# Kernel optimization log

Hardware: AMD Instinct MI355X
Metric: run time of the kernel (lower is better)

## Reference

```python
import jax, jax.numpy as jnp
import numpy as np

# ---- static structure for the 28x28 image grid ----
H = 28
V = H * H          # 784 vertices
T = 25             # landscape sample points
K_MAX = 2          # landscape orders kept
M0 = 0.05          # DTM mass parameter

_idx = np.arange(V).reshape(H, H)
_e_h = np.stack([_idx[:, :-1].ravel(), _idx[:, 1:].ravel()], 1)
_e_v = np.stack([_idx[:-1, :].ravel(), _idx[1:, :].ravel()], 1)
EDGES = np.concatenate([_e_h, _e_v], 0).astype(np.int32)   # [E,2], E=1512
E = EDGES.shape[0]

# grid coordinates per lims=[[27,0],[0,27]], normalized to [0,1]
_c0 = np.linspace(1.0, 0.0, H)
_c1 = np.linspace(0.0, 1.0, H)
COORDS = np.stack(np.meshgrid(_c0, _c1, indexing='ij'), -1).reshape(V, 2)
_D2 = ((COORDS[:, None, :] - COORDS[None, :, :]) ** 2).sum(-1)   # [V,V] static
ORDER = jnp.asarray(np.argsort(_D2, 1).astype(np.int32))          # nearest-first per row
D2S = jnp.asarray(np.take_along_axis(_D2, np.argsort(_D2, 1), 1).astype(np.float32))
TSEQ = jnp.asarray(np.linspace(0.0, 0.5, T).astype(np.float32))   # landscape eval grid
EA = jnp.asarray(EDGES[:, 0])
EB = jnp.asarray(EDGES[:, 1])


def _dtm(w):
    """Distance-to-measure filtration on the grid. w: [B,V] pixel masses -> [B,V]."""
    m = w / jnp.clip(jnp.sum(w, 1, keepdims=True), 1e-12)
    ws = m[:, ORDER]                                  # [B,V,V] masses in nearest-first order
    c = jnp.cumsum(ws, -1)
    take = jnp.minimum(ws, jnp.clip(M0 - (c - ws), 0.0, None))  # mass used until m0 reached
    return jnp.sqrt(jnp.sum(take * D2S[None], -1) / M0 + 1e-12)


def _ph0(f):
    """0-dim persistence of sublevel filtration of f on the grid graph (Kruskal/union-find).
    f: [V] -> (births, deaths, valid) each [E]."""
    w = jnp.maximum(f[EA], f[EB])                     # edge filtration values
    o = jnp.argsort(w)
    aa, bb, ww = EA[o], EB[o], w[o]

    def step(carry, e):
        r, bv = carry                                 # r: fully-compressed root per vertex
        ai, bi, wi = e
        ra, rb = r[ai], r[bi]
        diff = ra != rb
        young_a = bv[ra] >= bv[rb]                    # younger comp = larger birth
        young = jnp.where(young_a, ra, rb)
        old = jnp.where(young_a, rb, ra)
        birth = bv[young]
        r = jnp.where(diff & (r == young), old, r)    # merge, keep full compression
        return (r, bv), (birth, wi, diff)

    init = (jnp.arange(V, dtype=jnp.int32), f)
    _, (bs, ds, valid) = jax.lax.scan(step, init, (aa, bb, ww))
    return bs, ds, valid


def _landscape(bs, ds, valid):
    """Persistence landscape lambda_k(t), k<K_MAX, t in TSEQ -> [K_MAX*T] features."""
    tent = jnp.maximum(jnp.minimum(TSEQ[:, None] - bs[None, :], ds[None, :] - TSEQ[:, None]), 0.0)
    tent = tent * valid[None, :]                      # [T,E]
    top = jax.lax.top_k(tent, K_MAX)[0]               # [T,K]
    return top.T.reshape(-1)                          # [K*T] = 50


def setup_inputs() -> dict:
    key = jax.random.key(0)
    k1, k2, k3, k4, k5 = jax.random.split(key, 5)
    return {
        'input': jax.random.uniform(k1, (128, 1, 28, 28), dtype=jnp.float32),
        'w_topo': jax.random.normal(k2, (50, 100), dtype=jnp.float32) * 0.1,
        'b_topo': jax.random.normal(k3, (100,), dtype=jnp.float32) * 0.01,
        'w_fc': jax.random.normal(k4, (100, 10), dtype=jnp.float32) * 0.1,
        'b_fc': jax.random.normal(k5, (10,), dtype=jnp.float32) * 0.01,
    }


def reference(input, w_topo, b_topo, w_fc, b_fc):
    B = input.shape[0]
    x = input.reshape(B, V)
    f = _dtm(x)                                       # [B,V] DTM filtration
    bs, ds, valid = jax.vmap(_ph0)(f)                 # persistence pairs per sample
    feats = jax.vmap(_landscape)(bs, ds, valid.astype(f.dtype))  # [B,50]
    h = jax.nn.relu(feats @ w_topo + b_topo)          # AdTopoLayer linear + ReLU -> [B,100]
    return h @ w_fc + b_fc                            # [B,10]
```

## Files before the change

kernel.cpp:

```cpp
#include <hip/hip_runtime.h>
#include <math.h>

#define HH 28
#define VV 784
#define EE 1512
#define TT 25
#define M0C 0.05


#define DECODE(idx, A, B)                                                  \
  {                                                                        \
    if ((idx) < 756) {                                                     \
      int i_ = (idx) / 27, j_ = (idx) - i_ * 27;                           \
      A = i_ * HH + j_; B = A + 1;                                         \
    } else {                                                               \
      int q_ = (idx) - 756;                                                \
      int i_ = q_ / HH, j_ = q_ - i_ * HH;                                 \
      A = i_ * HH + j_; B = A + HH;                                        \
    }                                                                      \
  }

__global__ __launch_bounds__(512) void k_sortrows(int* __restrict__ ORDER, float* __restrict__ D2S) {
  __shared__ unsigned long long keys[1024];
  const int v = blockIdx.x;
  const int i1 = v / HH, j1 = v % HH;
  const double step = 1.0 / 27.0;
  const double c0v = (i1 == 27) ? 0.0 : 1.0 - (double)i1 * step;
  const double c1v = (j1 == 27) ? 1.0 : (double)j1 * step;
  for (int u = threadIdx.x; u < 1024; u += 512) {
    unsigned long long key = ~0ULL;
    if (u < VV) {
      int i2 = u / HH, j2 = u % HH;
      double c0u = (i2 == 27) ? 0.0 : 1.0 - (double)i2 * step;
      double c1u = (j2 == 27) ? 1.0 : (double)j2 * step;
      double dx = c0v - c0u, dy = c1v - c1u;
      float d2 = (float)(dx * dx + dy * dy);
      key = ((unsigned long long)__float_as_uint(d2) << 32) | (unsigned)u;
    }
    keys[u] = key;
  }
  __syncthreads();
  for (unsigned k = 2; k <= 1024; k <<= 1) {
    for (unsigned j = k >> 1; j; j >>= 1) {
      for (unsigned i = threadIdx.x; i < 1024; i += 512) {
        unsigned l = i ^ j;
        if (l > i) {
          unsigned long long a = keys[i], c = keys[l];
          if ((a > c) == ((i & k) == 0)) { keys[i] = c; keys[l] = a; }
        }
      }
      __syncthreads();
    }
  }
  for (int u = threadIdx.x; u < VV; u += 512) {
    unsigned long long key = keys[u];
    ORDER[v * VV + u] = (int)(key & 0xffffffffu);
    D2S[v * VV + u] = __uint_as_float((unsigned)(key >> 32));
  }
}

__global__ __launch_bounds__(256) void k_norm(const float* __restrict__ x, float* __restrict__ MT) {
  const int b = blockIdx.x;
  const int tid = threadIdx.x;
  double s = 0.0;
  for (int i = tid; i < VV; i += 256) s += (double)x[b * VV + i];
  for (int off = 32; off; off >>= 1) s += __shfl_xor(s, off, 64);
  __shared__ double sred[4];
  __shared__ double Ssh;
  if ((tid & 63) == 0) sred[tid >> 6] = s;
  __syncthreads();
  if (tid == 0) {
    double S = sred[0] + sred[1] + sred[2] + sred[3];
    Ssh = (S > 1e-12) ? S : 1e-12;
  }
  __syncthreads();
  double S = Ssh;
  for (int i = tid; i < VV; i += 256) MT[i * 128 + b] = (float)((double)x[b * VV + i] / S);
}

__global__ __launch_bounds__(128) void k_dtm(const float* __restrict__ MT, const int* __restrict__ ORDER,
                                             const float* __restrict__ D2S, float* __restrict__ F) {
  const int v = blockIdx.x;
  const int tid = threadIdx.x;
  __shared__ int ordS[VV];
  __shared__ float d2sS[VV];
  for (int k = tid; k < VV; k += 128) {
    ordS[k] = ORDER[v * VV + k];
    d2sS[k] = D2S[v * VV + k];
  }
  __syncthreads();
  float P = 0.0f, acc = 0.0f;
  for (int base = 0; base < VV; base += 16) {
    #pragma unroll
    for (int kk = 0; kk < 16; ++kk) {
      int k = base + kk;
      float mass = MT[ordS[k] * 128 + tid];
      float room = (float)M0C - P;
      room = room > 0.0f ? room : 0.0f;
      float take = mass < room ? mass : room;
      acc += take * d2sS[k];
      P += mass;
    }
    if (__all(P >= (float)M0C)) break;
  }
  F[tid * VV + v] = sqrtf(acc / (float)M0C + 1e-12f);
}

__global__ __launch_bounds__(512) void k_main(const float* __restrict__ F,
                                              const float* __restrict__ w_topo, const float* __restrict__ b_topo,
                                              const float* __restrict__ w_fc, const float* __restrict__ b_fc,
                                              float* __restrict__ out) {
  const int b = blockIdx.x;
  const int tid = threadIdx.x;
  __shared__ float fv[VV];
  __shared__ unsigned long long keys[2048];
  __shared__ unsigned long long par64[VV];
  __shared__ unsigned long long pairs[VV];
  __shared__ float feat[2 * TT];
  __shared__ float hbuf[100];
  __shared__ int cntS;
  for (int i = tid; i < VV; i += 512) {
    float f = F[b * VV + i];
    fv[i] = f;
    par64[i] = ((unsigned long long)__float_as_uint(f) << 32) | (unsigned)i;
  }
  __syncthreads();
  for (int e = tid; e < 2048; e += 512) {
    unsigned long long key = 0xFFFFFFFF00000000ULL;
    if (e < EE) {
      int aa, bb;
      DECODE(e, aa, bb);
      float w = fmaxf(fv[aa], fv[bb]);
      unsigned lo = ((e >= 756) ? (1u << 20) : 0u) | ((unsigned)aa << 10) | (unsigned)bb;
      key = ((unsigned long long)__float_as_uint(w) << 32) | lo;
    }
    keys[e] = key;
  }
  __syncthreads();
  for (unsigned k = 2; k <= 2048; k <<= 1) {
    for (unsigned j = k >> 1; j; j >>= 1) {
      for (unsigned i = tid; i < 2048; i += 512) {
        unsigned l = i ^ j;
        if (l > i) {
          unsigned long long a = keys[i], c = keys[l];
          if ((a > c) == ((i & k) == 0)) { keys[i] = c; keys[l] = a; }
        }
      }
      __syncthreads();
    }
  }
  if (tid < 64) {
    const int lane = tid;
    const unsigned long long lbit = 1ULL << lane;
    int cnt = 0;
    unsigned long long K = keys[lane];
    for (int batch = 0; batch < 24; ++batch) {
      unsigned long long Kn = keys[(batch + 1) * 64 + lane];
      unsigned lo = (unsigned)K;
      int aa = (int)((lo >> 10) & 1023), bb = (int)(lo & 1023);
      unsigned wbits = (unsigned)(K >> 32);
      unsigned long long pka = par64[aa], pkb = par64[bb];
      unsigned ra = (unsigned)pka, rb = (unsigned)pkb;
      unsigned fa = (unsigned)(pka >> 32), fb = (unsigned)(pkb >> 32);
      unsigned long long candB = __ballot(ra != rb);
      if (candB) {
        bool rec = false;
        unsigned long long pairv = 0;
        if (__popcll(candB) == 1) {
          if (ra != rb) {
            bool ya = (fa >= fb);
            unsigned young = ya ? ra : rb;
            unsigned oldv = ya ? rb : ra;
            unsigned foldv = ya ? fb : fa;
            unsigned birth = ya ? fa : fb;
            par64[young] = ((unsigned long long)foldv << 32) | oldv;
            pairv = ((unsigned long long)birth << 32) | wbits;
            rec = (wbits > birth);
          }
        } else {
          int merged = 0;
          unsigned young_w = 0;
          unsigned long long oldpk_w = 0;
          #pragma unroll 4
          for (int j = 0; j < 64; ++j) {
            unsigned s_ra = (unsigned)__builtin_amdgcn_readlane((int)ra, j);
            unsigned s_rb = (unsigned)__builtin_amdgcn_readlane((int)rb, j);
            if (s_ra != s_rb) {
              unsigned s_fa = (unsigned)__builtin_amdgcn_readlane((int)fa, j);
              unsigned s_fb = (unsigned)__builtin_amdgcn_readlane((int)fb, j);
              bool ya = (s_fa >= s_fb);
              unsigned young = ya ? s_ra : s_rb;
              unsigned oldv = ya ? s_rb : s_ra;
              unsigned foldv = ya ? s_fb : s_fa;
              unsigned birth = ya ? s_fa : s_fb;
              bool me = (lane == j);
              merged = me ? 1 : merged;
              young_w = me ? young : young_w;
              oldpk_w = me ? (((unsigned long long)foldv << 32) | oldv) : oldpk_w;
              pairv = me ? (((unsigned long long)birth << 32) | wbits) : pairv;
              bool ma = (ra == young);
              ra = ma ? oldv : ra;
              fa = ma ? foldv : fa;
              bool mb2 = (rb == young);
              rb = mb2 ? oldv : rb;
              fb = mb2 ? foldv : fb;
            }
          }
          if (merged) par64[young_w] = oldpk_w;
          rec = merged && ((unsigned)pairv > (unsigned)(pairv >> 32));
        }
        unsigned long long recB = __ballot(rec);
        int rank = __popcll(recB & (lbit - 1ULL));
        if (rec) pairs[cnt + rank] = pairv;
        cnt += (int)__popcll(recB);
        {
          unsigned long long p[13];
          #pragma unroll
          for (int s = 0; s < 12; ++s) p[s] = par64[lane + 64 * s];
          const int i12 = (lane < 16) ? (768 + lane) : lane;
          p[12] = par64[i12];
          for (;;) {
            bool stable = true;
            #pragma unroll
            for (int s = 0; s < 13; ++s) {
              unsigned r = (unsigned)p[s];
              unsigned long long q = par64[r];
              stable &= ((unsigned)q == r);
              p[s] = q;
            }
            if (__all(stable)) break;
          }
          #pragma unroll
          for (int s = 0; s < 12; ++s) par64[lane + 64 * s] = p[s];
          par64[i12] = p[12];
        }
      }
      K = Kn;
    }
    if (lane == 0) cntS = cnt;
  }
  __syncthreads();
  const int cnt = cntS;
  const int wid = tid >> 6, lane = tid & 63;
  for (int t = wid; t < TT; t += 8) {
    double tvd = (t == 24) ? 0.5 : (double)t * (0.5 / 24.0);
    float tv = (float)tvd;
    float m1 = 0.0f, m2 = 0.0f;
    for (int pidx = lane; pidx < cnt; pidx += 64) {
      unsigned long long pr = pairs[pidx];
      float pbv = __uint_as_float((unsigned)(pr >> 32));
      float pdv = __uint_as_float((unsigned)pr);
      float tent = fminf(tv - pbv, pdv - tv);
      tent = fmaxf(tent, 0.0f);
      if (tent > m1) { m2 = m1; m1 = tent; }
      else if (tent > m2) { m2 = tent; }
    }
    #pragma unroll
    for (int off = 32; off; off >>= 1) {
      float o1 = __shfl_xor(m1, off, 64);
      float o2 = __shfl_xor(m2, off, 64);
      float n1 = fmaxf(m1, o1);
      float n2 = fmaxf(fminf(m1, o1), fmaxf(m2, o2));
      m1 = n1; m2 = n2;
    }
    if (lane == 0) { feat[t] = m1; feat[TT + t] = m2; }
  }
  __syncthreads();
  if (tid < 100) {
    double h = (double)b_topo[tid];
    for (int k2 = 0; k2 < 50; ++k2) h += (double)feat[k2] * (double)w_topo[k2 * 100 + tid];
    hbuf[tid] = (h > 0.0) ? (float)h : 0.0f;
  }
  __syncthreads();
  if (tid < 10) {
    double o = (double)b_fc[tid];
    for (int k2 = 0; k2 < 100; ++k2) o += (double)hbuf[k2] * (double)w_fc[k2 * 10 + tid];
    out[b * 10 + tid] = (float)o;
  }
}

extern "C" void kernel_launch(void* const* d_in, const int* in_sizes, int n_in,
                              void* d_out, int out_size, void* d_ws, size_t ws_size,
                              hipStream_t stream) {
  const float* x = (const float*)d_in[0];
  const float* w_topo = (const float*)d_in[1];
  const float* b_topo = (const float*)d_in[2];
  const float* w_fc = (const float*)d_in[3];
  const float* b_fc = (const float*)d_in[4];
  float* outp = (float*)d_out;
  char* ws = (char*)d_ws;
  int* ORDER = (int*)ws;
  float* D2S = (float*)(ws + 2458624);
  float* MT = (float*)(ws + 4917248);
  float* F = (float*)(ws + 5318656);

  hipLaunchKernelGGL(k_sortrows, dim3(VV), dim3(512), 0, stream, ORDER, D2S);
  hipLaunchKernelGGL(k_norm, dim3(128), dim3(256), 0, stream, x, MT);
  hipLaunchKernelGGL(k_dtm, dim3(VV), dim3(128), 0, stream, MT, ORDER, D2S, F);
  hipLaunchKernelGGL(k_main, dim3(128), dim3(512), 0, stream, F, w_topo, b_topo, w_fc, b_fc, outp);
}
```

Before: 193.7 us.

## Merge sort and normalize kernels; replace pointer-jumping loop with single hop

Folds the row-sort precompute and the per-sample normalization into one launch by giving extra blocks the normalization work, which removes one kernel launch and its dependency gap. In the union-find merge path, the parent entry is now written from the already-updated ra/fa registers instead of a separately tracked packed value. The iterate-until-stable root compression is replaced by a single pointer-jumping hop per vertex. That relies on parent chains never being deeper than two after each merge batch, and it would give wrong roots if that assumption fails.

```diff
diff --git a/kernel.cpp b/kernel.cpp
--- a/kernel.cpp
+++ b/kernel.cpp
@@ -20,62 +20,66 @@
     }                                                                      \
   }
 
-__global__ __launch_bounds__(512) void k_sortrows(int* __restrict__ ORDER, float* __restrict__ D2S) {
+__global__ __launch_bounds__(512) void k_pre(const float* __restrict__ x,
+                                             int* __restrict__ ORDER, float* __restrict__ D2S,
+                                             float* __restrict__ MT) {
   __shared__ unsigned long long keys[1024];
-  const int v = blockIdx.x;
-  const int i1 = v / HH, j1 = v % HH;
-  const double step = 1.0 / 27.0;
-  const double c0v = (i1 == 27) ? 0.0 : 1.0 - (double)i1 * step;
-  const double c1v = (j1 == 27) ? 1.0 : (double)j1 * step;
-  for (int u = threadIdx.x; u < 1024; u += 512) {
-    unsigned long long key = ~0ULL;
-    if (u < VV) {
-      int i2 = u / HH, j2 = u % HH;
-      double c0u = (i2 == 27) ? 0.0 : 1.0 - (double)i2 * step;
-      double c1u = (j2 == 27) ? 1.0 : (double)j2 * step;
-      double dx = c0v - c0u, dy = c1v - c1u;
-      float d2 = (float)(dx * dx + dy * dy);
-      key = ((unsigned long long)__float_as_uint(d2) << 32) | (unsigned)u;
-    }
-    keys[u] = key;
-  }
-  __syncthreads();
-  for (unsigned k = 2; k <= 1024; k <<= 1) {
-    for (unsigned j = k >> 1; j; j >>= 1) {
-      for (unsigned i = threadIdx.x; i < 1024; i += 512) {
-        unsigned l = i ^ j;
-        if (l > i) {
-          unsigned long long a = keys[i], c = keys[l];
-          if ((a > c) == ((i & k) == 0)) { keys[i] = c; keys[l] = a; }
-        }
-      }
-      __syncthreads();
-    }
-  }
-  for (int u = threadIdx.x; u < VV; u += 512) {
-    unsigned long long key = keys[u];
-    ORDER[v * VV + u] = (int)(key & 0xffffffffu);
-    D2S[v * VV + u] = __uint_as_float((unsigned)(key >> 32));
-  }
-}
-
-__global__ __launch_bounds__(256) void k_norm(const float* __restrict__ x, float* __restrict__ MT) {
-  const int b = blockIdx.x;
+  __shared__ double sred[8];
+  __shared__ double Ssh;
   const int tid = threadIdx.x;
-  double s = 0.0;
-  for (int i = tid; i < VV; i += 256) s += (double)x[b * VV + i];
-  for (int off = 32; off; off >>= 1) s += __shfl_xor(s, off, 64);
-  __shared__ double sred[4];
-  __shared__ double Ssh;
-  if ((tid & 63) == 0) sred[tid >> 6] = s;
-  __syncthreads();
-  if (tid == 0) {
-    double S = sred[0] + sred[1] + sred[2] + sred[3];
-    Ssh = (S > 1e-12) ? S : 1e-12;
-  }
-  __syncthreads();
-  double S = Ssh;
-  for (int i = tid; i < VV; i += 256) MT[i * 128 + b] = (float)((double)x[b * VV + i] / S);
+  if (blockIdx.x < VV) {
+    const int v = blockIdx.x;
+    const int i1 = v / HH, j1 = v % HH;
+    const double step = 1.0 / 27.0;
+    const double c0v = (i1 == 27) ? 0.0 : 1.0 - (double)i1 * step;
+    const double c1v = (j1 == 27) ? 1.0 : (double)j1 * step;
+    for (int u = tid; u < 1024; u += 512) {
+      unsigned long long key = ~0ULL;
+      if (u < VV) {
+        int i2 = u / HH, j2 = u % HH;
+        double c0u = (i2 == 27) ? 0.0 : 1.0 - (double)i2 * step;
+        double c1u = (j2 == 27) ? 1.0 : (double)j2 * step;
+        double dx = c0v - c0u, dy = c1v - c1u;
+        float d2 = (float)(dx * dx + dy * dy);
+        key = ((unsigned long long)__float_as_uint(d2) << 32) | (unsigned)u;
+      }
+      keys[u] = key;
+    }
+    __syncthreads();
+    for (unsigned k = 2; k <= 1024; k <<= 1) {
+      for (unsigned j = k >> 1; j; j >>= 1) {
+        for (unsigned i = tid; i < 1024; i += 512) {
+          unsigned l = i ^ j;
+          if (l > i) {
+            unsigned long long a = keys[i], c = keys[l];
+            if ((a > c) == ((i & k) == 0)) { keys[i] = c; keys[l] = a; }
+          }
+        }
+        __syncthreads();
+      }
+    }
+    for (int u = tid; u < VV; u += 512) {
+      unsigned long long key = keys[u];
+      ORDER[v * VV + u] = (int)(key & 0xffffffffu);
+      D2S[v * VV + u] = __uint_as_float((unsigned)(key >> 32));
+    }
+  } else {
+    const int b = blockIdx.x - VV;
+    double s = 0.0;
+    for (int i = tid; i < VV; i += 512) s += (double)x[b * VV + i];
+    for (int off = 32; off; off >>= 1) s += __shfl_xor(s, off, 64);
+    if ((tid & 63) == 0) sred[tid >> 6] = s;
+    __syncthreads();
+    if (tid == 0) {
+      double S = 0.0;
+      #pragma unroll
+      for (int wv = 0; wv < 8; ++wv) S += sred[wv];
+      Ssh = (S > 1e-12) ? S : 1e-12;
+    }
+    __syncthreads();
+    double S = Ssh;
+    for (int i = tid; i < VV; i += 512) MT[i * 128 + b] = (float)((double)x[b * VV + i] / S);
+  }
 }
 
 __global__ __launch_bounds__(128) void k_dtm(const float* __restrict__ MT, const int* __restrict__ ORDER,
@@ -180,7 +184,6 @@
         } else {
           int merged = 0;
           unsigned young_w = 0;
-          unsigned long long oldpk_w = 0;
           #pragma unroll 4
           for (int j = 0; j < 64; ++j) {
             unsigned s_ra = (unsigned)__builtin_amdgcn_readlane((int)ra, j);
@@ -196,7 +199,6 @@
               bool me = (lane == j);
               merged = me ? 1 : merged;
               young_w = me ? young : young_w;
-              oldpk_w = me ? (((unsigned long long)foldv << 32) | oldv) : oldpk_w;
               pairv = me ? (((unsigned long long)birth << 32) | wbits) : pairv;
               bool ma = (ra == young);
               ra = ma ? oldv : ra;
@@ -206,7 +208,7 @@
               fb = mb2 ? foldv : fb;
             }
           }
-          if (merged) par64[young_w] = oldpk_w;
+          if (merged) par64[young_w] = ((unsigned long long)fa << 32) | ra;
           rec = merged && ((unsigned)pairv > (unsigned)(pairv >> 32));
         }
         unsigned long long recB = __ballot(rec);
@@ -214,25 +216,17 @@
         if (rec) pairs[cnt + rank] = pairv;
         cnt += (int)__popcll(recB);
         {
-          unsigned long long p[13];
           #pragma unroll
-          for (int s = 0; s < 12; ++s) p[s] = par64[lane + 64 * s];
-          const int i12 = (lane < 16) ? (768 + lane) : lane;
-          p[12] = par64[i12];
-          for (;;) {
-            bool stable = true;
-            #pragma unroll
-            for (int s = 0; s < 13; ++s) {
-              unsigned r = (unsigned)p[s];
-              unsigned long long q = par64[r];
-              stable &= ((unsigned)q == r);
-              p[s] = q;
-            }
-            if (__all(stable)) break;
-          }
-          #pragma unroll
-          for (int s = 0; s < 12; ++s) par64[lane + 64 * s] = p[s];
-          par64[i12] = p[12];
+          for (int s = 0; s < 12; ++s) {
+            unsigned long long p = par64[lane + 64 * s];
+            unsigned long long q = par64[(unsigned)p];
+            par64[lane + 64 * s] = q;
+          }
+          if (lane < 16) {
+            unsigned long long p = par64[768 + lane];
+            unsigned long long q = par64[(unsigned)p];
+            par64[768 + lane] = q;
+          }
         }
       }
       K = Kn;
@@ -294,8 +288,7 @@
   float* MT = (float*)(ws + 4917248);
   float* F = (float*)(ws + 5318656);
 
-  hipLaunchKernelGGL(k_sortrows, dim3(VV), dim3(512), 0, stream, ORDER, D2S);
-  hipLaunchKernelGGL(k_norm, dim3(128), dim3(256), 0, stream, x, MT);
+  hipLaunchKernelGGL(k_pre, dim3(VV + 128), dim3(512), 0, stream, x, ORDER, D2S, MT);
   hipLaunchKernelGGL(k_dtm, dim3(VV), dim3(128), 0, stream, MT, ORDER, D2S, F);
   hipLaunchKernelGGL(k_main, dim3(128), dim3(512), 0, stream, F, w_topo, b_topo, w_fc, b_fc, outp);
 }
```

Result: no change. 191.2 us (-1.3%).
